# Optimization experiments

Measured on AMD Instinct MI355X. Metric: run time of the kernel, lower is better.

Reference implementation:

```python
import jax, jax.numpy as jnp
import numpy as np

B, SQ, SK, D = 32, 2048, 2048, 64


def setup_inputs() -> dict:
    key = jax.random.key(0)
    kq, kk, km = jax.random.split(key, 3)
    q = jax.random.normal(kq, (B, SQ, D), dtype=jnp.float32)
    k = jax.random.normal(kk, (B, SK, D), dtype=jnp.float32)
    mask = jax.random.randint(km, (B, SQ, SK), 0, 2, dtype=jnp.int32)
    return {"q": q, "k": k, "mask": mask}


def reference(q, k, mask):
    # scores = q @ k^T / sqrt(D)  -> [B, SQ, SK]
    scale = 1.0 / np.sqrt(q.shape[-1]).astype(np.float32)
    scores = jnp.einsum('bqd,bkd->bqk', q, k) * scale
    scores = jnp.where(mask == 0, -jnp.inf, scores)
    return jax.nn.softmax(scores, axis=-1)
```

## Files before the change

kernel.cpp:

```cpp
#include <hip/hip_runtime.h>
#include <math.h>

constexpr int BB  = 32;
constexpr int SQL = 2048;
constexpr int SKL = 2048;
constexpr int DD  = 64;

using f32x4 = __attribute__((ext_vector_type(4))) float;
using bfrag = __attribute__((ext_vector_type(8))) short;
typedef unsigned long long u64;

static __device__ __forceinline__ unsigned short f2bf(float x) {
    unsigned u = __float_as_uint(x);
    u = u + 0x7FFFu + ((u >> 16) & 1u);
    return (unsigned short)(u >> 16);
}
static __device__ __forceinline__ float bf2f(unsigned short h) {
    return __uint_as_float((unsigned)h << 16);
}

static __device__ __forceinline__ void gld16(const void* g, void* l) {
    __builtin_amdgcn_global_load_lds(
        (const __attribute__((address_space(1))) void*)(size_t)g,
        (__attribute__((address_space(3))) void*)(unsigned)(size_t)l,
        16, 0, 0);
}

__global__ __launch_bounds__(256) void compress_mask(
    const int* __restrict__ m, unsigned char* __restrict__ bm)
{
    const int t = threadIdx.x;
    const size_t g0 = (size_t)blockIdx.x * 1024 + t;
    const int4* mp = (const int4*)m;
    int4 a0 = mp[(g0)       * 2], a1 = mp[(g0)       * 2 + 1];
    int4 b0 = mp[(g0 + 256) * 2], b1 = mp[(g0 + 256) * 2 + 1];
    int4 c0 = mp[(g0 + 512) * 2], c1 = mp[(g0 + 512) * 2 + 1];
    int4 d0 = mp[(g0 + 768) * 2], d1 = mp[(g0 + 768) * 2 + 1];
#define PACK8(v0, v1)                                                         \
    (unsigned char)((v0.x != 0 ? 1u : 0u)  | (v0.y != 0 ? 2u : 0u)   |        \
                    (v0.z != 0 ? 4u : 0u)  | (v0.w != 0 ? 8u : 0u)   |        \
                    (v1.x != 0 ? 16u : 0u) | (v1.y != 0 ? 32u : 0u)  |        \
                    (v1.z != 0 ? 64u : 0u) | (v1.w != 0 ? 128u : 0u))
    bm[g0]       = PACK8(a0, a1);
    bm[g0 + 256] = PACK8(b0, b1);
    bm[g0 + 512] = PACK8(c0, c1);
    bm[g0 + 768] = PACK8(d0, d1);
#undef PACK8
}

__global__ __launch_bounds__(256) void split_k_swz(
    const float* __restrict__ k, unsigned char* __restrict__ kswz)
{
    const int i0 = blockIdx.x * blockDim.x + threadIdx.x;
    const int g  = i0 & 7;
    const int c  = (i0 >> 3) & 2047;
    const int b  = i0 >> 14;
    const float* kp = k + ((size_t)(b * 2048 + c)) * DD + g * 8;
    bfrag h, lo;
    #pragma unroll
    for (int j = 0; j < 8; ++j) {
        const float x = kp[j];
        const unsigned short hh = f2bf(x);
        h[j]  = (short)hh;
        lo[j] = (short)f2bf(x - bf2f(hh));
    }
    const int sw = (c & 7) << 4;
    unsigned char* rec = kswz + ((size_t)(b * 2048 + c)) * 256;
    *(bfrag*)(rec + ((g * 16) ^ sw))       = h;
    *(bfrag*)(rec + 128 + ((g * 16) ^ sw)) = lo;
}

template<bool PRE>
__global__ __launch_bounds__(512, 4) void sdpa_v9(
    const float* __restrict__ q, const float* __restrict__ k,
    const int* __restrict__ mask, const unsigned char* __restrict__ bm,
    const unsigned char* __restrict__ kswz, float* __restrict__ out)
{
    __shared__ char klds[8][2][4096];
    __shared__ float s_red[8][16];

    const int t   = threadIdx.x;
    const int l   = t & 63;
    const int w   = t >> 6;
    const int lr  = l & 15;
    const int lg  = l >> 4;
    const int bid = blockIdx.x;
    const int swz = (bid & 7) * 512 + (bid >> 3);
    const int b   = swz >> 7;
    const int r0  = (swz & 127) * 16;
    const int c0  = w * 256;
    const size_t rowg = (size_t)b * SQL + (size_t)(r0 + lr);
    const int swk = (lr & 7) << 4;

    constexpr float QS = 0.18033688011112042f;
    bfrag qh0, ql0, qh1, ql1;
    {
        const float* qp = q + rowg * DD + lg * 8;
        const f32x4 x0 = *reinterpret_cast<const f32x4*>(qp);
        const f32x4 x1 = *reinterpret_cast<const f32x4*>(qp + 4);
        const f32x4 y0 = *reinterpret_cast<const f32x4*>(qp + 32);
        const f32x4 y1 = *reinterpret_cast<const f32x4*>(qp + 36);
        #pragma unroll
        for (int j = 0; j < 4; ++j) {
            float a = x0[j] * QS, c = x1[j] * QS;
            float d = y0[j] * QS, e = y1[j] * QS;
            unsigned short h;
            h = f2bf(a); qh0[j]     = (short)h; ql0[j]     = (short)f2bf(a - bf2f(h));
            h = f2bf(c); qh0[j + 4] = (short)h; ql0[j + 4] = (short)f2bf(c - bf2f(h));
            h = f2bf(d); qh1[j]     = (short)h; ql1[j]     = (short)f2bf(d - bf2f(h));
            h = f2bf(e); qh1[j + 4] = (short)h; ql1[j + 4] = (short)f2bf(e - bf2f(h));
        }
    }

    u64 mw0 = 0, mw1 = 0, mw2 = 0, mw3 = 0;
    if constexpr (PRE) {
        const ulonglong2* wp =
            (const ulonglong2*)(bm + rowg * (SKL / 8) + w * 32);
        const ulonglong2 v01 = wp[0];
        const ulonglong2 v23 = wp[1];
        mw0 = v01.x; mw1 = v01.y; mw2 = v23.x; mw3 = v23.y;
    }

    const char*  ksrc = PRE ? (const char*)(kswz + (size_t)b * SKL * 256) : nullptr;
    const float* kraw = PRE ? nullptr : k + (size_t)b * SKL * DD;
    const int*   mrp  = PRE ? nullptr : mask + rowg * SKL + c0 + lg * 4;
    char* seg = &klds[w][0][0];

#define STAGE(T)                                                               \
    do {                                                                       \
        char* _d = seg + (((T) & 1) << 12);                                    \
        if constexpr (PRE) {                                                   \
            const char* _s = ksrc + (size_t)(c0 + (T) * 16) * 256;             \
            gld16(_s + l * 16,        _d + l * 16);                            \
            gld16(_s + 1024 + l * 16, _d + 1024 + l * 16);                     \
            gld16(_s + 2048 + l * 16, _d + 2048 + l * 16);                     \
            gld16(_s + 3072 + l * 16, _d + 3072 + l * 16);                     \
        } else {                                                               \
            const float* _kc = kraw + (size_t)(c0 + (T) * 16 + lr) * DD;       \
            const f32x4 _a0 = *(const f32x4*)(_kc + lg * 8);                   \
            const f32x4 _a1 = *(const f32x4*)(_kc + lg * 8 + 4);               \
            const f32x4 _b0 = *(const f32x4*)(_kc + (lg + 4) * 8);             \
            const f32x4 _b1 = *(const f32x4*)(_kc + (lg + 4) * 8 + 4);         \
            bfrag _h, _o;                                                      \
            _Pragma("unroll")                                                  \
            for (int _j = 0; _j < 4; ++_j) {                                   \
                unsigned short _t;                                             \
                _t = f2bf(_a0[_j]); _h[_j]   = (short)_t;                      \
                _o[_j]   = (short)f2bf(_a0[_j] - bf2f(_t));                    \
                _t = f2bf(_a1[_j]); _h[_j+4] = (short)_t;                      \
                _o[_j+4] = (short)f2bf(_a1[_j] - bf2f(_t));                    \
            }                                                                  \
            char* _rec = _d + lr * 256;                                        \
            *(bfrag*)(_rec + ((lg * 16) ^ swk))       = _h;                    \
            *(bfrag*)(_rec + 128 + ((lg * 16) ^ swk)) = _o;                    \
            _Pragma("unroll")                                                  \
            for (int _j = 0; _j < 4; ++_j) {                                   \
                unsigned short _t;                                             \
                _t = f2bf(_b0[_j]); _h[_j]   = (short)_t;                      \
                _o[_j]   = (short)f2bf(_b0[_j] - bf2f(_t));                    \
                _t = f2bf(_b1[_j]); _h[_j+4] = (short)_t;                      \
                _o[_j+4] = (short)f2bf(_b1[_j] - bf2f(_t));                    \
            }                                                                  \
            *(bfrag*)(_rec + (((lg + 4) * 16) ^ swk))       = _h;              \
            *(bfrag*)(_rec + 128 + (((lg + 4) * 16) ^ swk)) = _o;              \
        }                                                                      \
    } while (0)

#define ITER(T, VMC, MW)                                                       \
    do {                                                                       \
        if constexpr (PRE)                                                     \
            asm volatile("s_waitcnt vmcnt(" #VMC ")" ::: "memory");            \
        const char* _c = seg + (((T) & 1) << 12) + lr * 256;                   \
        const bfrag _kh0 = *(const bfrag*)(_c + ((lg * 16) ^ swk));            \
        const bfrag _kh1 = *(const bfrag*)(_c + (((lg + 4) * 16) ^ swk));      \
        const bfrag _kl0 = *(const bfrag*)(_c + 128 + ((lg * 16) ^ swk));      \
        const bfrag _kl1 = *(const bfrag*)(_c + 128 + (((lg + 4) * 16) ^ swk));\
        asm volatile("s_waitcnt lgkmcnt(0)" ::: "memory");                     \
        __builtin_amdgcn_sched_barrier(0);                                     \
        if constexpr ((T) + 2 < 16) STAGE((T) + 2);                            \
        int4 _mv;                                                              \
        if constexpr (!PRE) _mv = *(const int4*)(mrp + (T) * 16);              \
        f32x4 _a1 = {0.f, 0.f, 0.f, 0.f};                                      \
        f32x4 _a2 = {0.f, 0.f, 0.f, 0.f};                                      \
        f32x4 _a3 = {0.f, 0.f, 0.f, 0.f};                                      \
        _a1 = __builtin_amdgcn_mfma_f32_16x16x32_bf16(_kl0, qh0, _a1, 0, 0, 0);\
        _a2 = __builtin_amdgcn_mfma_f32_16x16x32_bf16(_kh0, ql0, _a2, 0, 0, 0);\
        _a3 = __builtin_amdgcn_mfma_f32_16x16x32_bf16(_kh0, qh0, _a3, 0, 0, 0);\
        _a1 = __builtin_amdgcn_mfma_f32_16x16x32_bf16(_kl1, qh1, _a1, 0, 0, 0);\
        _a2 = __builtin_amdgcn_mfma_f32_16x16x32_bf16(_kh1, ql1, _a2, 0, 0, 0);\
        _a3 = __builtin_amdgcn_mfma_f32_16x16x32_bf16(_kh1, qh1, _a3, 0, 0, 0);\
        const f32x4 _s = (_a1 + _a2) + _a3;                                    \
        unsigned _nib;                                                         \
        if constexpr (PRE)                                                     \
            _nib = (unsigned)((MW) >> (((T) & 3) * 16 + lg * 4)) & 0xFu;       \
        else                                                                   \
            _nib = (_mv.x != 0 ? 1u : 0u) | (_mv.y != 0 ? 2u : 0u)             \
                 | (_mv.z != 0 ? 4u : 0u) | (_mv.w != 0 ? 8u : 0u);            \
        const float _e0 = (_nib & 1u) ? exp2f(_s[0]) : 0.f;                    \
        const float _e1 = (_nib & 2u) ? exp2f(_s[1]) : 0.f;                    \
        const float _e2 = (_nib & 4u) ? exp2f(_s[2]) : 0.f;                    \
        const float _e3 = (_nib & 8u) ? exp2f(_s[3]) : 0.f;                    \
        psum += (_e0 + _e1) + (_e2 + _e3);                                     \
        sc[2 * (T)    ] = (unsigned)f2bf(_e0) | ((unsigned)f2bf(_e1) << 16);   \
        sc[2 * (T) + 1] = (unsigned)f2bf(_e2) | ((unsigned)f2bf(_e3) << 16);   \
    } while (0)

    unsigned sc[32];
    float psum = 0.f;

    STAGE(0);
    STAGE(1);

    ITER(0,  4, mw0); ITER(1,  4, mw0); ITER(2,  4, mw0); ITER(3,  4, mw0);
    ITER(4,  4, mw1); ITER(5,  4, mw1); ITER(6,  4, mw1); ITER(7,  4, mw1);
    ITER(8,  4, mw2); ITER(9,  4, mw2); ITER(10, 4, mw2); ITER(11, 4, mw2);
    ITER(12, 4, mw3); ITER(13, 4, mw3); ITER(14, 4, mw3); ITER(15, 0, mw3);
#undef ITER
#undef STAGE

    float s = psum;
    s += __shfl_xor(s, 16, 64);
    s += __shfl_xor(s, 32, 64);
    if (l < 16) s_red[w][lr] = s;
    __syncthreads();

    float tot = 0.f;
    #pragma unroll
    for (int ww = 0; ww < 8; ++ww)
        tot += s_red[ww][lr];
    const float rinv = 1.0f / tot;

    float* op = out + rowg * SKL + c0 + lg * 4;
    #pragma unroll
    for (int T = 0; T < 16; ++T) {
        const unsigned p01 = sc[2 * T];
        const unsigned p23 = sc[2 * T + 1];
        f32x4 o;
        o[0] = bf2f((unsigned short)(p01 & 0xffffu)) * rinv;
        o[1] = bf2f((unsigned short)(p01 >> 16))     * rinv;
        o[2] = bf2f((unsigned short)(p23 & 0xffffu)) * rinv;
        o[3] = bf2f((unsigned short)(p23 >> 16))     * rinv;
        *reinterpret_cast<f32x4*>(op + T * 16) = o;
    }
}

extern "C" void kernel_launch(void* const* d_in, const int* in_sizes, int n_in,
                              void* d_out, int out_size, void* d_ws, size_t ws_size,
                              hipStream_t stream) {
    const float* q    = (const float*)d_in[0];
    const float* k    = (const float*)d_in[1];
    const int*   mask = (const int*)d_in[2];
    float*       out  = (float*)d_out;

    const size_t BM_B = (size_t)BB * SQL * SKL / 8;
    const size_t KS_B = (size_t)BB * SKL * 256;

    dim3 grid(4096);

    if (ws_size >= BM_B + KS_B) {
        unsigned char* bmp = (unsigned char*)d_ws;
        unsigned char* ksp = (unsigned char*)d_ws + BM_B;
        compress_mask<<<16384, 256, 0, stream>>>(mask, bmp);
        split_k_swz<<<2048, 256, 0, stream>>>(k, ksp);
        sdpa_v9<true><<<grid, 512, 0, stream>>>(q, k, mask, bmp, ksp, out);
    } else {
        sdpa_v9<false><<<grid, 512, 0, stream>>>(q, k, mask, nullptr, nullptr, out);
    }
}
```

Baseline: 344.0 us.

## Drop mask compression pass; stream raw mask tiles into LDS via async loads

Removes the separate compress_mask kernel, which read the full int32 mask and wrote a bitmask that the main kernel then reread. The main kernel now streams raw int32 mask tiles into a swizzled double-buffered LDS region with global_load_lds, alongside the K tiles, and reads them back per iteration. This cuts one full extra pass over the mask and a kernel launch. In exchange LDS use per block rises to 80KB, which may lower occupancy, and the vmcnt wait counts are retuned to account for the extra load per stage.

```diff
diff --git a/kernel.cpp b/kernel.cpp
--- a/kernel.cpp
+++ b/kernel.cpp
@@ -8,7 +8,6 @@
 
 using f32x4 = __attribute__((ext_vector_type(4))) float;
 using bfrag = __attribute__((ext_vector_type(8))) short;
-typedef unsigned long long u64;
 
 static __device__ __forceinline__ unsigned short f2bf(float x) {
     unsigned u = __float_as_uint(x);
@@ -24,28 +23,6 @@
         (const __attribute__((address_space(1))) void*)(size_t)g,
         (__attribute__((address_space(3))) void*)(unsigned)(size_t)l,
         16, 0, 0);
-}
-
-__global__ __launch_bounds__(256) void compress_mask(
-    const int* __restrict__ m, unsigned char* __restrict__ bm)
-{
-    const int t = threadIdx.x;
-    const size_t g0 = (size_t)blockIdx.x * 1024 + t;
-    const int4* mp = (const int4*)m;
-    int4 a0 = mp[(g0)       * 2], a1 = mp[(g0)       * 2 + 1];
-    int4 b0 = mp[(g0 + 256) * 2], b1 = mp[(g0 + 256) * 2 + 1];
-    int4 c0 = mp[(g0 + 512) * 2], c1 = mp[(g0 + 512) * 2 + 1];
-    int4 d0 = mp[(g0 + 768) * 2], d1 = mp[(g0 + 768) * 2 + 1];
-#define PACK8(v0, v1)                                                         \
-    (unsigned char)((v0.x != 0 ? 1u : 0u)  | (v0.y != 0 ? 2u : 0u)   |        \
-                    (v0.z != 0 ? 4u : 0u)  | (v0.w != 0 ? 8u : 0u)   |        \
-                    (v1.x != 0 ? 16u : 0u) | (v1.y != 0 ? 32u : 0u)  |        \
-                    (v1.z != 0 ? 64u : 0u) | (v1.w != 0 ? 128u : 0u))
-    bm[g0]       = PACK8(a0, a1);
-    bm[g0 + 256] = PACK8(b0, b1);
-    bm[g0 + 512] = PACK8(c0, c1);
-    bm[g0 + 768] = PACK8(d0, d1);
-#undef PACK8
 }
 
 __global__ __launch_bounds__(256) void split_k_swz(
@@ -71,13 +48,12 @@
 }
 
 template<bool PRE>
-__global__ __launch_bounds__(512, 4) void sdpa_v9(
+__global__ __launch_bounds__(512, 4) void sdpa_v10(
     const float* __restrict__ q, const float* __restrict__ k,
-    const int* __restrict__ mask, const unsigned char* __restrict__ bm,
-    const unsigned char* __restrict__ kswz, float* __restrict__ out)
+    const int* __restrict__ mask, const unsigned char* __restrict__ kswz,
+    float* __restrict__ out)
 {
-    __shared__ char klds[8][2][4096];
-    __shared__ float s_red[8][16];
+    __shared__ char pool[81920];
 
     const int t   = threadIdx.x;
     const int l   = t & 63;
@@ -91,6 +67,9 @@
     const int c0  = w * 256;
     const size_t rowg = (size_t)b * SQL + (size_t)(r0 + lr);
     const int swk = (lr & 7) << 4;
+
+    char* kseg = pool + w * 10240;
+    char* mseg = kseg + 8192;
 
     constexpr float QS = 0.18033688011112042f;
     bfrag qh0, ql0, qh1, ql1;
@@ -112,29 +91,24 @@
         }
     }
 
-    u64 mw0 = 0, mw1 = 0, mw2 = 0, mw3 = 0;
-    if constexpr (PRE) {
-        const ulonglong2* wp =
-            (const ulonglong2*)(bm + rowg * (SKL / 8) + w * 32);
-        const ulonglong2 v01 = wp[0];
-        const ulonglong2 v23 = wp[1];
-        mw0 = v01.x; mw1 = v01.y; mw2 = v23.x; mw3 = v23.y;
-    }
-
-    const char*  ksrc = PRE ? (const char*)(kswz + (size_t)b * SKL * 256) : nullptr;
+    const char* ksrc = PRE ? (const char*)(kswz + (size_t)b * SKL * 256) : nullptr;
     const float* kraw = PRE ? nullptr : k + (size_t)b * SKL * DD;
-    const int*   mrp  = PRE ? nullptr : mask + rowg * SKL + c0 + lg * 4;
-    char* seg = &klds[w][0][0];
+
+    const int* msrc = mask + ((size_t)b * SQL + (size_t)(r0 + (l >> 2))) * SKL
+                           + c0 + (((l & 3) ^ ((l >> 3) & 3)) << 2);
+    const int moff = lr * 64 + ((lg ^ ((lr >> 1) & 3)) << 4);
+    const int* mrp = PRE ? nullptr : mask + rowg * SKL + c0 + lg * 4;
 
 #define STAGE(T)                                                               \
     do {                                                                       \
-        char* _d = seg + (((T) & 1) << 12);                                    \
+        char* _kd = kseg + (((T) & 1) << 12);                                  \
         if constexpr (PRE) {                                                   \
-            const char* _s = ksrc + (size_t)(c0 + (T) * 16) * 256;             \
-            gld16(_s + l * 16,        _d + l * 16);                            \
-            gld16(_s + 1024 + l * 16, _d + 1024 + l * 16);                     \
-            gld16(_s + 2048 + l * 16, _d + 2048 + l * 16);                     \
-            gld16(_s + 3072 + l * 16, _d + 3072 + l * 16);                     \
+            const char* _ks = ksrc + (size_t)(c0 + (T) * 16) * 256;            \
+            gld16(_ks + l * 16,        _kd + l * 16);                          \
+            gld16(_ks + 1024 + l * 16, _kd + 1024 + l * 16);                   \
+            gld16(_ks + 2048 + l * 16, _kd + 2048 + l * 16);                   \
+            gld16(_ks + 3072 + l * 16, _kd + 3072 + l * 16);                   \
+            gld16(msrc + (T) * 16, mseg + (((T) & 1) << 10) + l * 16);         \
         } else {                                                               \
             const float* _kc = kraw + (size_t)(c0 + (T) * 16 + lr) * DD;       \
             const f32x4 _a0 = *(const f32x4*)(_kc + lg * 8);                   \
@@ -150,7 +124,7 @@
                 _t = f2bf(_a1[_j]); _h[_j+4] = (short)_t;                      \
                 _o[_j+4] = (short)f2bf(_a1[_j] - bf2f(_t));                    \
             }                                                                  \
-            char* _rec = _d + lr * 256;                                        \
+            char* _rec = _kd + lr * 256;                                       \
             *(bfrag*)(_rec + ((lg * 16) ^ swk))       = _h;                    \
             *(bfrag*)(_rec + 128 + ((lg * 16) ^ swk)) = _o;                    \
             _Pragma("unroll")                                                  \
@@ -166,20 +140,23 @@
         }                                                                      \
     } while (0)
 
-#define ITER(T, VMC, MW)                                                       \
+#define ITER(T, VMC)                                                           \
     do {                                                                       \
         if constexpr (PRE)                                                     \
             asm volatile("s_waitcnt vmcnt(" #VMC ")" ::: "memory");            \
-        const char* _c = seg + (((T) & 1) << 12) + lr * 256;                   \
+        const char* _c = kseg + (((T) & 1) << 12) + lr * 256;                  \
         const bfrag _kh0 = *(const bfrag*)(_c + ((lg * 16) ^ swk));            \
         const bfrag _kh1 = *(const bfrag*)(_c + (((lg + 4) * 16) ^ swk));      \
         const bfrag _kl0 = *(const bfrag*)(_c + 128 + ((lg * 16) ^ swk));      \
         const bfrag _kl1 = *(const bfrag*)(_c + 128 + (((lg + 4) * 16) ^ swk));\
+        int4 _mv;                                                              \
+        if constexpr (PRE)                                                     \
+            _mv = *(const int4*)(mseg + (((T) & 1) << 10) + moff);             \
+        else                                                                   \
+            _mv = *(const int4*)(mrp + (T) * 16);                              \
         asm volatile("s_waitcnt lgkmcnt(0)" ::: "memory");                     \
         __builtin_amdgcn_sched_barrier(0);                                     \
         if constexpr ((T) + 2 < 16) STAGE((T) + 2);                            \
-        int4 _mv;                                                              \
-        if constexpr (!PRE) _mv = *(const int4*)(mrp + (T) * 16);              \
         f32x4 _a1 = {0.f, 0.f, 0.f, 0.f};                                      \
         f32x4 _a2 = {0.f, 0.f, 0.f, 0.f};                                      \
         f32x4 _a3 = {0.f, 0.f, 0.f, 0.f};                                      \
@@ -190,16 +167,10 @@
         _a2 = __builtin_amdgcn_mfma_f32_16x16x32_bf16(_kh1, ql1, _a2, 0, 0, 0);\
         _a3 = __builtin_amdgcn_mfma_f32_16x16x32_bf16(_kh1, qh1, _a3, 0, 0, 0);\
         const f32x4 _s = (_a1 + _a2) + _a3;                                    \
-        unsigned _nib;                                                         \
-        if constexpr (PRE)                                                     \
-            _nib = (unsigned)((MW) >> (((T) & 3) * 16 + lg * 4)) & 0xFu;       \
-        else                                                                   \
-            _nib = (_mv.x != 0 ? 1u : 0u) | (_mv.y != 0 ? 2u : 0u)             \
-                 | (_mv.z != 0 ? 4u : 0u) | (_mv.w != 0 ? 8u : 0u);            \
-        const float _e0 = (_nib & 1u) ? exp2f(_s[0]) : 0.f;                    \
-        const float _e1 = (_nib & 2u) ? exp2f(_s[1]) : 0.f;                    \
-        const float _e2 = (_nib & 4u) ? exp2f(_s[2]) : 0.f;                    \
-        const float _e3 = (_nib & 8u) ? exp2f(_s[3]) : 0.f;                    \
+        const float _e0 = (_mv.x != 0) ? exp2f(_s[0]) : 0.f;                   \
+        const float _e1 = (_mv.y != 0) ? exp2f(_s[1]) : 0.f;                   \
+        const float _e2 = (_mv.z != 0) ? exp2f(_s[2]) : 0.f;                   \
+        const float _e3 = (_mv.w != 0) ? exp2f(_s[3]) : 0.f;                   \
         psum += (_e0 + _e1) + (_e2 + _e3);                                     \
         sc[2 * (T)    ] = (unsigned)f2bf(_e0) | ((unsigned)f2bf(_e1) << 16);   \
         sc[2 * (T) + 1] = (unsigned)f2bf(_e2) | ((unsigned)f2bf(_e3) << 16);   \
@@ -211,23 +182,26 @@
     STAGE(0);
     STAGE(1);
 
-    ITER(0,  4, mw0); ITER(1,  4, mw0); ITER(2,  4, mw0); ITER(3,  4, mw0);
-    ITER(4,  4, mw1); ITER(5,  4, mw1); ITER(6,  4, mw1); ITER(7,  4, mw1);
-    ITER(8,  4, mw2); ITER(9,  4, mw2); ITER(10, 4, mw2); ITER(11, 4, mw2);
-    ITER(12, 4, mw3); ITER(13, 4, mw3); ITER(14, 4, mw3); ITER(15, 0, mw3);
+    ITER(0,  5); ITER(1,  5); ITER(2,  5); ITER(3,  5);
+    ITER(4,  5); ITER(5,  5); ITER(6,  5); ITER(7,  5);
+    ITER(8,  5); ITER(9,  5); ITER(10, 5); ITER(11, 5);
+    ITER(12, 5); ITER(13, 5); ITER(14, 5); ITER(15, 0);
 #undef ITER
 #undef STAGE
 
     float s = psum;
     s += __shfl_xor(s, 16, 64);
     s += __shfl_xor(s, 32, 64);
-    if (l < 16) s_red[w][lr] = s;
+
+    __syncthreads();
+    float* s_red = (float*)pool;
+    if (l < 16) s_red[w * 16 + lr] = s;
     __syncthreads();
 
     float tot = 0.f;
     #pragma unroll
     for (int ww = 0; ww < 8; ++ww)
-        tot += s_red[ww][lr];
+        tot += s_red[ww * 16 + lr];
     const float rinv = 1.0f / tot;
 
     float* op = out + rowg * SKL + c0 + lg * 4;
@@ -252,18 +226,15 @@
     const int*   mask = (const int*)d_in[2];
     float*       out  = (float*)d_out;
 
-    const size_t BM_B = (size_t)BB * SQL * SKL / 8;
     const size_t KS_B = (size_t)BB * SKL * 256;
 
     dim3 grid(4096);
 
-    if (ws_size >= BM_B + KS_B) {
-        unsigned char* bmp = (unsigned char*)d_ws;
-        unsigned char* ksp = (unsigned char*)d_ws + BM_B;
-        compress_mask<<<16384, 256, 0, stream>>>(mask, bmp);
+    if (ws_size >= KS_B) {
+        unsigned char* ksp = (unsigned char*)d_ws;
         split_k_swz<<<2048, 256, 0, stream>>>(k, ksp);
-        sdpa_v9<true><<<grid, 512, 0, stream>>>(q, k, mask, bmp, ksp, out);
+        sdpa_v10<true><<<grid, 512, 0, stream>>>(q, k, mask, ksp, out);
     } else {
-        sdpa_v9<false><<<grid, 512, 0, stream>>>(q, k, mask, nullptr, nullptr, out);
-    }
-}
+        sdpa_v10<false><<<grid, 512, 0, stream>>>(q, k, mask, nullptr, out);
+    }
+}
```

New measurement: 352.5 us. +2.5%, slower.

## Process two 16-row query tiles per block to reuse staged K fragments

Applied to the files above, without the earlier changes.

Each block now handles 32 query rows instead of 16, so every K tile staged in LDS feeds two sets of MFMAs. The grid is halved and the K staging moves from a double buffer to a triple buffer with a deeper prefetch distance. The bf16 packing of the exponentials now uses an inline v_cvt_pk_bf16_f32 instruction. The intent is to halve K traffic per query row and hide load latency better, at the cost of more registers (sc grows to 64), lower occupancy bounds (launch_bounds min blocks 4 to 2), and more LDS per block.

```diff
diff --git a/kernel.cpp b/kernel.cpp
--- a/kernel.cpp
+++ b/kernel.cpp
@@ -71,13 +71,12 @@
 }
 
 template<bool PRE>
-__global__ __launch_bounds__(512, 4) void sdpa_v9(
+__global__ __launch_bounds__(512, 2) void sdpa_v13(
     const float* __restrict__ q, const float* __restrict__ k,
     const int* __restrict__ mask, const unsigned char* __restrict__ bm,
     const unsigned char* __restrict__ kswz, float* __restrict__ out)
 {
-    __shared__ char klds[8][2][4096];
-    __shared__ float s_red[8][16];
+    __shared__ char pool[8 * 12288 + 1024];
 
     const int t   = threadIdx.x;
     const int l   = t & 63;
@@ -85,56 +84,29 @@
     const int lr  = l & 15;
     const int lg  = l >> 4;
     const int bid = blockIdx.x;
-    const int swz = (bid & 7) * 512 + (bid >> 3);
-    const int b   = swz >> 7;
-    const int r0  = (swz & 127) * 16;
+    const int swz = (bid & 7) * 256 + (bid >> 3);
+    const int b   = swz >> 6;
+    const int r0  = (swz & 63) * 32;
     const int c0  = w * 256;
-    const size_t rowg = (size_t)b * SQL + (size_t)(r0 + lr);
+    const size_t row0 = (size_t)b * SQL + (size_t)(r0 + lr);
+    const size_t row1 = row0 + 16;
     const int swk = (lr & 7) << 4;
 
-    constexpr float QS = 0.18033688011112042f;
-    bfrag qh0, ql0, qh1, ql1;
-    {
-        const float* qp = q + rowg * DD + lg * 8;
-        const f32x4 x0 = *reinterpret_cast<const f32x4*>(qp);
-        const f32x4 x1 = *reinterpret_cast<const f32x4*>(qp + 4);
-        const f32x4 y0 = *reinterpret_cast<const f32x4*>(qp + 32);
-        const f32x4 y1 = *reinterpret_cast<const f32x4*>(qp + 36);
-        #pragma unroll
-        for (int j = 0; j < 4; ++j) {
-            float a = x0[j] * QS, c = x1[j] * QS;
-            float d = y0[j] * QS, e = y1[j] * QS;
-            unsigned short h;
-            h = f2bf(a); qh0[j]     = (short)h; ql0[j]     = (short)f2bf(a - bf2f(h));
-            h = f2bf(c); qh0[j + 4] = (short)h; ql0[j + 4] = (short)f2bf(c - bf2f(h));
-            h = f2bf(d); qh1[j]     = (short)h; ql1[j]     = (short)f2bf(d - bf2f(h));
-            h = f2bf(e); qh1[j + 4] = (short)h; ql1[j + 4] = (short)f2bf(e - bf2f(h));
-        }
-    }
-
-    u64 mw0 = 0, mw1 = 0, mw2 = 0, mw3 = 0;
-    if constexpr (PRE) {
-        const ulonglong2* wp =
-            (const ulonglong2*)(bm + rowg * (SKL / 8) + w * 32);
-        const ulonglong2 v01 = wp[0];
-        const ulonglong2 v23 = wp[1];
-        mw0 = v01.x; mw1 = v01.y; mw2 = v23.x; mw3 = v23.y;
-    }
-
-    const char*  ksrc = PRE ? (const char*)(kswz + (size_t)b * SKL * 256) : nullptr;
+    char* kseg = pool + w * 12288;
+    const char*  ksrc = PRE ? (const char*)(kswz + ((size_t)b * SKL + c0) * 256) : nullptr;
     const float* kraw = PRE ? nullptr : k + (size_t)b * SKL * DD;
-    const int*   mrp  = PRE ? nullptr : mask + rowg * SKL + c0 + lg * 4;
-    char* seg = &klds[w][0][0];
+    const int*   mr0  = PRE ? nullptr : mask + row0 * SKL + c0 + lg * 4;
+    const int*   mr1  = PRE ? nullptr : mask + row1 * SKL + c0 + lg * 4;
 
 #define STAGE(T)                                                               \
     do {                                                                       \
-        char* _d = seg + (((T) & 1) << 12);                                    \
+        char* _kd = kseg + ((T) % 3) * 4096;                                   \
         if constexpr (PRE) {                                                   \
-            const char* _s = ksrc + (size_t)(c0 + (T) * 16) * 256;             \
-            gld16(_s + l * 16,        _d + l * 16);                            \
-            gld16(_s + 1024 + l * 16, _d + 1024 + l * 16);                     \
-            gld16(_s + 2048 + l * 16, _d + 2048 + l * 16);                     \
-            gld16(_s + 3072 + l * 16, _d + 3072 + l * 16);                     \
+            const char* _ks = ksrc + (size_t)(T) * 4096;                       \
+            gld16(_ks + l * 16,        _kd + l * 16);                          \
+            gld16(_ks + 1024 + l * 16, _kd + 1024 + l * 16);                   \
+            gld16(_ks + 2048 + l * 16, _kd + 2048 + l * 16);                   \
+            gld16(_ks + 3072 + l * 16, _kd + 3072 + l * 16);                   \
         } else {                                                               \
             const float* _kc = kraw + (size_t)(c0 + (T) * 16 + lr) * DD;       \
             const f32x4 _a0 = *(const f32x4*)(_kc + lg * 8);                   \
@@ -144,103 +116,189 @@
             bfrag _h, _o;                                                      \
             _Pragma("unroll")                                                  \
             for (int _j = 0; _j < 4; ++_j) {                                   \
-                unsigned short _t;                                             \
-                _t = f2bf(_a0[_j]); _h[_j]   = (short)_t;                      \
-                _o[_j]   = (short)f2bf(_a0[_j] - bf2f(_t));                    \
-                _t = f2bf(_a1[_j]); _h[_j+4] = (short)_t;                      \
-                _o[_j+4] = (short)f2bf(_a1[_j] - bf2f(_t));                    \
+                unsigned short _t2;                                            \
+                _t2 = f2bf(_a0[_j]); _h[_j]   = (short)_t2;                    \
+                _o[_j]   = (short)f2bf(_a0[_j] - bf2f(_t2));                   \
+                _t2 = f2bf(_a1[_j]); _h[_j+4] = (short)_t2;                    \
+                _o[_j+4] = (short)f2bf(_a1[_j] - bf2f(_t2));                   \
             }                                                                  \
-            char* _rec = _d + lr * 256;                                        \
+            char* _rec = _kd + lr * 256;                                       \
             *(bfrag*)(_rec + ((lg * 16) ^ swk))       = _h;                    \
             *(bfrag*)(_rec + 128 + ((lg * 16) ^ swk)) = _o;                    \
             _Pragma("unroll")                                                  \
             for (int _j = 0; _j < 4; ++_j) {                                   \
-                unsigned short _t;                                             \
-                _t = f2bf(_b0[_j]); _h[_j]   = (short)_t;                      \
-                _o[_j]   = (short)f2bf(_b0[_j] - bf2f(_t));                    \
-                _t = f2bf(_b1[_j]); _h[_j+4] = (short)_t;                      \
-                _o[_j+4] = (short)f2bf(_b1[_j] - bf2f(_t));                    \
+                unsigned short _t2;                                            \
+                _t2 = f2bf(_b0[_j]); _h[_j]   = (short)_t2;                    \
+                _o[_j]   = (short)f2bf(_b0[_j] - bf2f(_t2));                   \
+                _t2 = f2bf(_b1[_j]); _h[_j+4] = (short)_t2;                    \
+                _o[_j+4] = (short)f2bf(_b1[_j] - bf2f(_t2));                   \
             }                                                                  \
             *(bfrag*)(_rec + (((lg + 4) * 16) ^ swk))       = _h;              \
             *(bfrag*)(_rec + 128 + (((lg + 4) * 16) ^ swk)) = _o;              \
         }                                                                      \
     } while (0)
 
-#define ITER(T, VMC, MW)                                                       \
+    STAGE(0);
+
+    constexpr float QS = 0.18033688011112042f;
+    bfrag qh0a, ql0a, qh1a, ql1a;
+    bfrag qh0b, ql0b, qh1b, ql1b;
+#define LOADQ(ROW, H0, L0, H1, L1)                                             \
+    do {                                                                       \
+        const float* _qp = q + (ROW) * DD + lg * 8;                            \
+        const f32x4 _x0 = *(const f32x4*)_qp;                                  \
+        const f32x4 _x1 = *(const f32x4*)(_qp + 4);                            \
+        const f32x4 _y0 = *(const f32x4*)(_qp + 32);                           \
+        const f32x4 _y1 = *(const f32x4*)(_qp + 36);                           \
+        _Pragma("unroll")                                                      \
+        for (int _j = 0; _j < 4; ++_j) {                                       \
+            float _a = _x0[_j] * QS, _c = _x1[_j] * QS;                        \
+            float _d = _y0[_j] * QS, _e = _y1[_j] * QS;                        \
+            unsigned short _h;                                                 \
+            _h = f2bf(_a); H0[_j]   = (short)_h; L0[_j]   = (short)f2bf(_a - bf2f(_h)); \
+            _h = f2bf(_c); H0[_j+4] = (short)_h; L0[_j+4] = (short)f2bf(_c - bf2f(_h)); \
+            _h = f2bf(_d); H1[_j]   = (short)_h; L1[_j]   = (short)f2bf(_d - bf2f(_h)); \
+            _h = f2bf(_e); H1[_j+4] = (short)_h; L1[_j+4] = (short)f2bf(_e - bf2f(_h)); \
+        }                                                                      \
+    } while (0)
+    LOADQ(row0, qh0a, ql0a, qh1a, ql1a);
+    LOADQ(row1, qh0b, ql0b, qh1b, ql1b);
+#undef LOADQ
+
+    u64 ma0 = 0, ma1 = 0, ma2 = 0, ma3 = 0;
+    u64 mb0 = 0, mb1 = 0, mb2 = 0, mb3 = 0;
+    if constexpr (PRE) {
+        const ulonglong2* wpa = (const ulonglong2*)(bm + row0 * (SKL / 8) + w * 32);
+        const ulonglong2* wpb = (const ulonglong2*)(bm + row1 * (SKL / 8) + w * 32);
+        const ulonglong2 va0 = wpa[0], va1 = wpa[1];
+        const ulonglong2 vb0 = wpb[0], vb1 = wpb[1];
+        ma0 = va0.x; ma1 = va0.y; ma2 = va1.x; ma3 = va1.y;
+        mb0 = vb0.x; mb1 = vb0.y; mb2 = vb1.x; mb3 = vb1.y;
+    }
+
+    STAGE(1);
+    STAGE(2);
+
+    unsigned sc[64];
+    float psum0 = 0.f, psum1 = 0.f;
+
+#define ITER(T, VMC, MA, MB)                                                   \
     do {                                                                       \
         if constexpr (PRE)                                                     \
             asm volatile("s_waitcnt vmcnt(" #VMC ")" ::: "memory");            \
-        const char* _c = seg + (((T) & 1) << 12) + lr * 256;                   \
+        const char* _c = kseg + ((T) % 3) * 4096 + lr * 256;                   \
         const bfrag _kh0 = *(const bfrag*)(_c + ((lg * 16) ^ swk));            \
         const bfrag _kh1 = *(const bfrag*)(_c + (((lg + 4) * 16) ^ swk));      \
         const bfrag _kl0 = *(const bfrag*)(_c + 128 + ((lg * 16) ^ swk));      \
         const bfrag _kl1 = *(const bfrag*)(_c + 128 + (((lg + 4) * 16) ^ swk));\
+        int4 _mva, _mvb;                                                       \
+        if constexpr (!PRE) {                                                  \
+            _mva = *(const int4*)(mr0 + (T) * 16);                             \
+            _mvb = *(const int4*)(mr1 + (T) * 16);                             \
+        }                                                                      \
         asm volatile("s_waitcnt lgkmcnt(0)" ::: "memory");                     \
         __builtin_amdgcn_sched_barrier(0);                                     \
-        if constexpr ((T) + 2 < 16) STAGE((T) + 2);                            \
-        int4 _mv;                                                              \
-        if constexpr (!PRE) _mv = *(const int4*)(mrp + (T) * 16);              \
-        f32x4 _a1 = {0.f, 0.f, 0.f, 0.f};                                      \
-        f32x4 _a2 = {0.f, 0.f, 0.f, 0.f};                                      \
-        f32x4 _a3 = {0.f, 0.f, 0.f, 0.f};                                      \
-        _a1 = __builtin_amdgcn_mfma_f32_16x16x32_bf16(_kl0, qh0, _a1, 0, 0, 0);\
-        _a2 = __builtin_amdgcn_mfma_f32_16x16x32_bf16(_kh0, ql0, _a2, 0, 0, 0);\
-        _a3 = __builtin_amdgcn_mfma_f32_16x16x32_bf16(_kh0, qh0, _a3, 0, 0, 0);\
-        _a1 = __builtin_amdgcn_mfma_f32_16x16x32_bf16(_kl1, qh1, _a1, 0, 0, 0);\
-        _a2 = __builtin_amdgcn_mfma_f32_16x16x32_bf16(_kh1, ql1, _a2, 0, 0, 0);\
-        _a3 = __builtin_amdgcn_mfma_f32_16x16x32_bf16(_kh1, qh1, _a3, 0, 0, 0);\
-        const f32x4 _s = (_a1 + _a2) + _a3;                                    \
-        unsigned _nib;                                                         \
-        if constexpr (PRE)                                                     \
-            _nib = (unsigned)((MW) >> (((T) & 3) * 16 + lg * 4)) & 0xFu;       \
-        else                                                                   \
-            _nib = (_mv.x != 0 ? 1u : 0u) | (_mv.y != 0 ? 2u : 0u)             \
-                 | (_mv.z != 0 ? 4u : 0u) | (_mv.w != 0 ? 8u : 0u);            \
-        const float _e0 = (_nib & 1u) ? exp2f(_s[0]) : 0.f;                    \
-        const float _e1 = (_nib & 2u) ? exp2f(_s[1]) : 0.f;                    \
-        const float _e2 = (_nib & 4u) ? exp2f(_s[2]) : 0.f;                    \
-        const float _e3 = (_nib & 8u) ? exp2f(_s[3]) : 0.f;                    \
-        psum += (_e0 + _e1) + (_e2 + _e3);                                     \
-        sc[2 * (T)    ] = (unsigned)f2bf(_e0) | ((unsigned)f2bf(_e1) << 16);   \
-        sc[2 * (T) + 1] = (unsigned)f2bf(_e2) | ((unsigned)f2bf(_e3) << 16);   \
+        if constexpr ((T) + 3 < 16) STAGE((T) + 3);                            \
+                                          \
+        f32x4 _h = {0.f, 0.f, 0.f, 0.f};                                       \
+        f32x4 _m = {0.f, 0.f, 0.f, 0.f};                                       \
+        _h = __builtin_amdgcn_mfma_f32_16x16x32_bf16(_kh0, qh0a, _h, 0, 0, 0); \
+        _m = __builtin_amdgcn_mfma_f32_16x16x32_bf16(_kh0, ql0a, _m, 0, 0, 0); \
+        _h = __builtin_amdgcn_mfma_f32_16x16x32_bf16(_kh1, qh1a, _h, 0, 0, 0); \
+        _m = __builtin_amdgcn_mfma_f32_16x16x32_bf16(_kl0, qh0a, _m, 0, 0, 0); \
+        _m = __builtin_amdgcn_mfma_f32_16x16x32_bf16(_kh1, ql1a, _m, 0, 0, 0); \
+        _m = __builtin_amdgcn_mfma_f32_16x16x32_bf16(_kl1, qh1a, _m, 0, 0, 0); \
+        const f32x4 _s0 = _h + _m;                                             \
+                                                                  \
+        f32x4 _h2 = {0.f, 0.f, 0.f, 0.f};                                      \
+        f32x4 _m2 = {0.f, 0.f, 0.f, 0.f};                                      \
+        _h2 = __builtin_amdgcn_mfma_f32_16x16x32_bf16(_kh0, qh0b, _h2, 0, 0, 0);\
+        _m2 = __builtin_amdgcn_mfma_f32_16x16x32_bf16(_kh0, ql0b, _m2, 0, 0, 0);\
+        _h2 = __builtin_amdgcn_mfma_f32_16x16x32_bf16(_kh1, qh1b, _h2, 0, 0, 0);\
+        _m2 = __builtin_amdgcn_mfma_f32_16x16x32_bf16(_kl0, qh0b, _m2, 0, 0, 0);\
+        _m2 = __builtin_amdgcn_mfma_f32_16x16x32_bf16(_kh1, ql1b, _m2, 0, 0, 0);\
+        _m2 = __builtin_amdgcn_mfma_f32_16x16x32_bf16(_kl1, qh1b, _m2, 0, 0, 0);\
+        const f32x4 _s1 = _h2 + _m2;                                           \
+        unsigned _n0, _n1;                                                     \
+        if constexpr (PRE) {                                                   \
+            _n0 = (unsigned)((MA) >> (((T) & 3) * 16 + lg * 4)) & 0xFu;        \
+            _n1 = (unsigned)((MB) >> (((T) & 3) * 16 + lg * 4)) & 0xFu;        \
+        } else {                                                               \
+            _n0 = (_mva.x != 0 ? 1u : 0u) | (_mva.y != 0 ? 2u : 0u)            \
+                | (_mva.z != 0 ? 4u : 0u) | (_mva.w != 0 ? 8u : 0u);           \
+            _n1 = (_mvb.x != 0 ? 1u : 0u) | (_mvb.y != 0 ? 2u : 0u)            \
+                | (_mvb.z != 0 ? 4u : 0u) | (_mvb.w != 0 ? 8u : 0u);           \
+        }                                                                      \
+        const float _e0 = (_n0 & 1u) ? exp2f(_s0[0]) : 0.f;                    \
+        const float _e1 = (_n0 & 2u) ? exp2f(_s0[1]) : 0.f;                    \
+        const float _e2 = (_n0 & 4u) ? exp2f(_s0[2]) : 0.f;                    \
+        const float _e3 = (_n0 & 8u) ? exp2f(_s0[3]) : 0.f;                    \
+        const float _f0 = (_n1 & 1u) ? exp2f(_s1[0]) : 0.f;                    \
+        const float _f1 = (_n1 & 2u) ? exp2f(_s1[1]) : 0.f;                    \
+        const float _f2 = (_n1 & 4u) ? exp2f(_s1[2]) : 0.f;                    \
+        const float _f3 = (_n1 & 8u) ? exp2f(_s1[3]) : 0.f;                    \
+        psum0 += (_e0 + _e1) + (_e2 + _e3);                                    \
+        psum1 += (_f0 + _f1) + (_f2 + _f3);                                    \
+        asm volatile("v_cvt_pk_bf16_f32 %0, %1, %2"                            \
+                     : "=v"(sc[4 * (T)])     : "v"(_e0), "v"(_e1));            \
+        asm volatile("v_cvt_pk_bf16_f32 %0, %1, %2"                            \
+                     : "=v"(sc[4 * (T) + 1]) : "v"(_e2), "v"(_e3));            \
+        asm volatile("v_cvt_pk_bf16_f32 %0, %1, %2"                            \
+                     : "=v"(sc[4 * (T) + 2]) : "v"(_f0), "v"(_f1));            \
+        asm volatile("v_cvt_pk_bf16_f32 %0, %1, %2"                            \
+                     : "=v"(sc[4 * (T) + 3]) : "v"(_f2), "v"(_f3));            \
     } while (0)
 
-    unsigned sc[32];
-    float psum = 0.f;
-
-    STAGE(0);
-    STAGE(1);
-
-    ITER(0,  4, mw0); ITER(1,  4, mw0); ITER(2,  4, mw0); ITER(3,  4, mw0);
-    ITER(4,  4, mw1); ITER(5,  4, mw1); ITER(6,  4, mw1); ITER(7,  4, mw1);
-    ITER(8,  4, mw2); ITER(9,  4, mw2); ITER(10, 4, mw2); ITER(11, 4, mw2);
-    ITER(12, 4, mw3); ITER(13, 4, mw3); ITER(14, 4, mw3); ITER(15, 0, mw3);
+    ITER(0,  8, ma0, mb0); ITER(1,  8, ma0, mb0);
+    ITER(2,  8, ma0, mb0); ITER(3,  8, ma0, mb0);
+    ITER(4,  8, ma1, mb1); ITER(5,  8, ma1, mb1);
+    ITER(6,  8, ma1, mb1); ITER(7,  8, ma1, mb1);
+    ITER(8,  8, ma2, mb2); ITER(9,  8, ma2, mb2);
+    ITER(10, 8, ma2, mb2); ITER(11, 8, ma2, mb2);
+    ITER(12, 8, ma3, mb3); ITER(13, 8, ma3, mb3);
+    ITER(14, 4, ma3, mb3); ITER(15, 0, ma3, mb3);
 #undef ITER
 #undef STAGE
 
-    float s = psum;
-    s += __shfl_xor(s, 16, 64);
-    s += __shfl_xor(s, 32, 64);
-    if (l < 16) s_red[w][lr] = s;
+    psum0 += __shfl_xor(psum0, 16, 64);
+    psum0 += __shfl_xor(psum0, 32, 64);
+    psum1 += __shfl_xor(psum1, 16, 64);
+    psum1 += __shfl_xor(psum1, 32, 64);
+
+    float* s_red = (float*)(pool + 8 * 12288);
     __syncthreads();
-
-    float tot = 0.f;
+    if (l < 16) {
+        s_red[w * 32 + lr]      = psum0;
+        s_red[w * 32 + 16 + lr] = psum1;
+    }
+    __syncthreads();
+
+    float tot0 = 0.f, tot1 = 0.f;
     #pragma unroll
-    for (int ww = 0; ww < 8; ++ww)
-        tot += s_red[ww][lr];
-    const float rinv = 1.0f / tot;
-
-    float* op = out + rowg * SKL + c0 + lg * 4;
+    for (int ww = 0; ww < 8; ++ww) {
+        tot0 += s_red[ww * 32 + lr];
+        tot1 += s_red[ww * 32 + 16 + lr];
+    }
+    const float rinv0 = 1.0f / tot0;
+    const float rinv1 = 1.0f / tot1;
+
+    float* op0 = out + row0 * SKL + c0 + lg * 4;
+    float* op1 = out + row1 * SKL + c0 + lg * 4;
     #pragma unroll
     for (int T = 0; T < 16; ++T) {
-        const unsigned p01 = sc[2 * T];
-        const unsigned p23 = sc[2 * T + 1];
-        f32x4 o;
-        o[0] = bf2f((unsigned short)(p01 & 0xffffu)) * rinv;
-        o[1] = bf2f((unsigned short)(p01 >> 16))     * rinv;
-        o[2] = bf2f((unsigned short)(p23 & 0xffffu)) * rinv;
-        o[3] = bf2f((unsigned short)(p23 >> 16))     * rinv;
-        *reinterpret_cast<f32x4*>(op + T * 16) = o;
+        const unsigned pa = sc[4 * T], pb = sc[4 * T + 1];
+        const unsigned pc = sc[4 * T + 2], pd = sc[4 * T + 3];
+        f32x4 o0, o1;
+        o0[0] = bf2f((unsigned short)(pa & 0xffffu)) * rinv0;
+        o0[1] = bf2f((unsigned short)(pa >> 16))     * rinv0;
+        o0[2] = bf2f((unsigned short)(pb & 0xffffu)) * rinv0;
+        o0[3] = bf2f((unsigned short)(pb >> 16))     * rinv0;
+        o1[0] = bf2f((unsigned short)(pc & 0xffffu)) * rinv1;
+        o1[1] = bf2f((unsigned short)(pc >> 16))     * rinv1;
+        o1[2] = bf2f((unsigned short)(pd & 0xffffu)) * rinv1;
+        o1[3] = bf2f((unsigned short)(pd >> 16))     * rinv1;
+        *reinterpret_cast<f32x4*>(op0 + T * 16) = o0;
+        *reinterpret_cast<f32x4*>(op1 + T * 16) = o1;
     }
 }
 
@@ -255,15 +313,15 @@
     const size_t BM_B = (size_t)BB * SQL * SKL / 8;
     const size_t KS_B = (size_t)BB * SKL * 256;
 
-    dim3 grid(4096);
+    dim3 grid(2048);
 
     if (ws_size >= BM_B + KS_B) {
         unsigned char* bmp = (unsigned char*)d_ws;
         unsigned char* ksp = (unsigned char*)d_ws + BM_B;
         compress_mask<<<16384, 256, 0, stream>>>(mask, bmp);
         split_k_swz<<<2048, 256, 0, stream>>>(k, ksp);
-        sdpa_v9<true><<<grid, 512, 0, stream>>>(q, k, mask, bmp, ksp, out);
+        sdpa_v13<true><<<grid, 512, 0, stream>>>(q, k, mask, bmp, ksp, out);
     } else {
-        sdpa_v9<false><<<grid, 512, 0, stream>>>(q, k, mask, nullptr, nullptr, out);
-    }
-}
+        sdpa_v13<false><<<grid, 512, 0, stream>>>(q, k, mask, nullptr, nullptr, out);
+    }
+}
```

Measured after the change: 335.7 us. 2.4% less time.
